# Kernel optimization log

Hardware: AMD Instinct MI355X
Metric: run time of the kernel (lower is better)

Reference implementation:

```python
import jax, jax.numpy as jnp
import numpy as np

N, IN_F, OUT_F = 2048, 512, 512

def setup_inputs() -> dict:
    key = jax.random.key(0)
    kx, ka, kb = jax.random.split(key, 3)
    x = jax.random.uniform(kx, (N, IN_F), dtype=jnp.float32)          # inputs in [0,1]
    a = jax.random.uniform(ka, (OUT_F, IN_F), dtype=jnp.float32)      # weight in [0,1]
    b = jax.random.uniform(kb, (OUT_F,), dtype=jnp.float32)           # bias in [0,1]
    return {"x": x, "a": a, "b": b}

def reference(x, a, b):
    # Lukasiewicz / max-plus 'matmul':
    # y[n,o] = max(0, max_i(x[n,i] + a[o,i] - 1)), then max with bias b[o].
    inter = x[:, None, :] + a[None, :, :] - 1.0        # [N, out, in]
    y = jnp.maximum(jnp.max(inter, axis=-1), 0.0)      # [N, out]
    y = jnp.maximum(y, b[None, :])
    return y
```

## Files before the change

### kernel.cpp

```cpp
#include <hip/hip_runtime.h>
#include <cstdint>


#define NROW 2048
#define NK   512
#define NCOL 512
#define RPB  8
#define CBL  256
#define KQ   32
typedef float f32x4 __attribute__((ext_vector_type(4)));

__device__ __forceinline__ void async_load16(const float* g, float* l) {
  __builtin_amdgcn_global_load_lds(
      (const __attribute__((address_space(1))) void*)g,
      (__attribute__((address_space(3))) void*)l, 16, 0, 0);
}

__global__ __launch_bounds__(256) void luka_prep(const float* __restrict__ A,
                                                 f32x4* __restrict__ Apb) {
  int idx = blockIdx.x * 256 + threadIdx.x;
  int o  = idx >> 7;
  int k4 = idx & 127;
  f32x4 v = *(const f32x4*)(A + o * NK + k4 * 4);
  Apb[(((o >> 8) * 128) + k4) * 256 + (o & 255)] = v;
}

__global__ __launch_bounds__(256, 2) void luka_main(
    const f32x4* __restrict__ Apb, const float* __restrict__ X,
    const float* __restrict__ Bv, float* __restrict__ Y) {
  __shared__ float xsl[RPB * NK];
  __shared__ float red[4 * RPB * CBL];
  const int tid  = threadIdx.x;
  const int lane = tid & 63;
  const int w    = tid >> 6;
  const int colblk  = blockIdx.x;
  const int rowBase = blockIdx.y * RPB;

  {
    const float* Xg = X + (size_t)rowBase * NK;
#pragma unroll
    for (int rnd = 0; rnd < 4; ++rnd) {
      int base = rnd * 256 + w * 64;
      async_load16(Xg + (size_t)(base + lane) * 4, &xsl[base * 4]);
    }
  }

  const f32x4* __restrict__ Aw =
      Apb + ((size_t)(colblk * 128 + w * KQ) * 256 + lane);

  float acc[RPB][4];
#pragma unroll
  for (int r = 0; r < RPB; ++r)
#pragma unroll
    for (int c = 0; c < 4; ++c) acc[r][c] = 0.0f;

  f32x4 a0 = Aw[0], a1 = Aw[64], a2 = Aw[128], a3 = Aw[192];

  __syncthreads();

#pragma unroll 2
  for (int j = 0; j < KQ; ++j) {
    f32x4 n0, n1, n2, n3;
    if (j + 1 < KQ) {
      n0 = Aw[(j + 1) * 256];
      n1 = Aw[(j + 1) * 256 + 64];
      n2 = Aw[(j + 1) * 256 + 128];
      n3 = Aw[(j + 1) * 256 + 192];
    }
    const int kb = (w * KQ + j) * 4;
#pragma unroll
    for (int r = 0; r < RPB; ++r) {
      const f32x4 xv = *(const f32x4*)&xsl[r * NK + kb];
      f32x4 s0 = a0 + xv;
      f32x4 s1 = a1 + xv;
      f32x4 s2 = a2 + xv;
      f32x4 s3 = a3 + xv;
      acc[r][0] = fmaxf(fmaxf(s0.x, s0.y), acc[r][0]);
      acc[r][0] = fmaxf(fmaxf(s0.z, s0.w), acc[r][0]);
      acc[r][1] = fmaxf(fmaxf(s1.x, s1.y), acc[r][1]);
      acc[r][1] = fmaxf(fmaxf(s1.z, s1.w), acc[r][1]);
      acc[r][2] = fmaxf(fmaxf(s2.x, s2.y), acc[r][2]);
      acc[r][2] = fmaxf(fmaxf(s2.z, s2.w), acc[r][2]);
      acc[r][3] = fmaxf(fmaxf(s3.x, s3.y), acc[r][3]);
      acc[r][3] = fmaxf(fmaxf(s3.z, s3.w), acc[r][3]);
    }
    a0 = n0; a1 = n1; a2 = n2; a3 = n3;
  }

#pragma unroll
  for (int r = 0; r < RPB; ++r)
#pragma unroll
    for (int c = 0; c < 4; ++c)
      red[(w * RPB + r) * CBL + c * 64 + lane] = acc[r][c];
  __syncthreads();

  const float bv = Bv[colblk * CBL + tid];
#pragma unroll
  for (int p = 0; p < RPB; ++p) {
    float m = fmaxf(fmaxf(red[(0 * RPB + p) * CBL + tid],
                          red[(1 * RPB + p) * CBL + tid]),
                    fmaxf(red[(2 * RPB + p) * CBL + tid],
                          red[(3 * RPB + p) * CBL + tid]));
    float t = m - 1.0f;
    Y[(size_t)(rowBase + p) * NCOL + colblk * CBL + tid] =
        fmaxf(fmaxf(t, bv), 0.0f);
  }
}

#define TILE 64
#define BK   64
__global__ __launch_bounds__(256) void luka_fb(
    const float* __restrict__ X, const float* __restrict__ A,
    const float* __restrict__ Bv, float* __restrict__ Y) {
  __shared__ float xs[2][TILE * BK];
  __shared__ float as[2][TILE * BK];
  const int tid = threadIdx.x, wave = tid >> 6, tx = tid & 15, ty = tid >> 4;
  const int rowBase = blockIdx.y * TILE, colBase = blockIdx.x * TILE;
  uint32_t xoff[4], aoff[4];
#pragma unroll
  for (int r = 0; r < 4; ++r) {
    int row = ty * 4 + r;
    xoff[r] = (uint32_t)row * 256u + ((uint32_t)((row & 15) ^ (row >> 2)) << 4);
  }
#pragma unroll
  for (int c = 0; c < 4; ++c) {
    int row = tx * 4 + c;
    aoff[c] = (uint32_t)row * 256u + ((uint32_t)((row & 15) ^ (row >> 2)) << 4);
  }
  float acc[4][4];
#pragma unroll
  for (int r = 0; r < 4; ++r)
#pragma unroll
    for (int c = 0; c < 4; ++c) acc[r][c] = 0.0f;
  const int row0 = tid >> 4, sl = tid & 15;
  auto stage = [&](int buf, int kt) {
#pragma unroll
    for (int j = 0; j < 4; ++j) {
      int row = row0 + j * 16;
      int m = (row & 15) ^ (row >> 2);
      int kk = ((sl ^ m) << 2);
      async_load16(X + (size_t)(rowBase + row) * NK + kt * BK + kk,
                   &xs[buf][j * 1024 + wave * 256]);
      async_load16(A + (size_t)(colBase + row) * NK + kt * BK + kk,
                   &as[buf][j * 1024 + wave * 256]);
    }
  };
  stage(0, 0);
  __syncthreads();
  int buf = 0;
#pragma unroll 1
  for (int kt = 0; kt < NK / BK; ++kt) {
    if (kt < NK / BK - 1) stage(buf ^ 1, kt + 1);
    const char* xb = (const char*)&xs[buf][0];
    const char* ab = (const char*)&as[buf][0];
#pragma unroll
    for (int s4 = 0; s4 < BK / 4; ++s4) {
      f32x4 xf[4], af[4];
#pragma unroll
      for (int r = 0; r < 4; ++r)
        xf[r] = *(const f32x4*)(xb + (xoff[r] ^ (uint32_t)(s4 << 4)));
#pragma unroll
      for (int c = 0; c < 4; ++c)
        af[c] = *(const f32x4*)(ab + (aoff[c] ^ (uint32_t)(s4 << 4)));
#pragma unroll
      for (int r = 0; r < 4; ++r)
#pragma unroll
        for (int c = 0; c < 4; ++c) {
          f32x4 s = xf[r] + af[c];
          float t0 = fmaxf(fmaxf(s.x, s.y), acc[r][c]);
          acc[r][c] = fmaxf(fmaxf(s.z, s.w), t0);
        }
    }
    __syncthreads();
    buf ^= 1;
  }
  const f32x4 bv = *(const f32x4*)&Bv[colBase + tx * 4];
  float bvv[4] = {bv.x, bv.y, bv.z, bv.w};
#pragma unroll
  for (int r = 0; r < 4; ++r) {
    f32x4 o;
    o.x = fmaxf(fmaxf(acc[r][0] - 1.0f, bvv[0]), 0.0f);
    o.y = fmaxf(fmaxf(acc[r][1] - 1.0f, bvv[1]), 0.0f);
    o.z = fmaxf(fmaxf(acc[r][2] - 1.0f, bvv[2]), 0.0f);
    o.w = fmaxf(fmaxf(acc[r][3] - 1.0f, bvv[3]), 0.0f);
    *(f32x4*)&Y[(size_t)(rowBase + ty * 4 + r) * NCOL + colBase + tx * 4] = o;
  }
}

extern "C" void kernel_launch(void* const* d_in, const int* in_sizes, int n_in,
                              void* d_out, int out_size, void* d_ws, size_t ws_size,
                              hipStream_t stream) {
  const float* X = (const float*)d_in[0];
  const float* A = (const float*)d_in[1];
  const float* B = (const float*)d_in[2];
  float* Y = (float*)d_out;

  if (ws_size >= (size_t)NCOL * NK * sizeof(float)) {
    f32x4* Apb = (f32x4*)d_ws;
    luka_prep<<<dim3(NCOL * NK / 4 / 256), dim3(256), 0, stream>>>(A, Apb);
    dim3 grid(NCOL / CBL, NROW / RPB);
    luka_main<<<grid, dim3(256), 0, stream>>>(Apb, X, B, Y);
  } else {
    dim3 grid(NCOL / TILE, NROW / TILE);
    luka_fb<<<grid, dim3(256), 0, stream>>>(X, A, B, Y);
  }
}
```

Before: 83.75 us.

## Interleave prepacked weight columns per lane and use nontemporal loads

The prep kernel now stores the four column-chunks each lane needs next to each other, so every thread reads 64 contiguous bytes per k-step instead of four strided 16-byte vectors. The main kernel reads the weights with nontemporal loads and drops the min-blocks-per-CU launch bound. This aims to cut memory transactions and cache pollution on the weight stream. The per-wave access becomes a 64-byte stride per lane, which may coalesce less well, and nontemporal hints may hurt reuse of A across row blocks.

```diff
diff --git a/kernel.cpp b/kernel.cpp
--- a/kernel.cpp
+++ b/kernel.cpp
@@ -17,16 +17,18 @@
 }
 
 __global__ __launch_bounds__(256) void luka_prep(const float* __restrict__ A,
-                                                 f32x4* __restrict__ Apb) {
+                                                 f32x4* __restrict__ Apc) {
   int idx = blockIdx.x * 256 + threadIdx.x;
   int o  = idx >> 7;
   int k4 = idx & 127;
+  int cb = o >> 8, oc = o & 255;
+  int c  = oc >> 6, l = oc & 63;
   f32x4 v = *(const f32x4*)(A + o * NK + k4 * 4);
-  Apb[(((o >> 8) * 128) + k4) * 256 + (o & 255)] = v;
-}
-
-__global__ __launch_bounds__(256, 2) void luka_main(
-    const f32x4* __restrict__ Apb, const float* __restrict__ X,
+  Apc[((cb * 128 + k4) << 8) + (l << 2) + c] = v;
+}
+
+__global__ __launch_bounds__(256) void luka_main(
+    const f32x4* __restrict__ Apc, const float* __restrict__ X,
     const float* __restrict__ Bv, float* __restrict__ Y) {
   __shared__ float xsl[RPB * NK];
   __shared__ float red[4 * RPB * CBL];
@@ -46,7 +48,7 @@
   }
 
   const f32x4* __restrict__ Aw =
-      Apb + ((size_t)(colblk * 128 + w * KQ) * 256 + lane);
+      Apc + (((size_t)(colblk * 128 + w * KQ)) << 8) + (lane << 2);
 
   float acc[RPB][4];
 #pragma unroll
@@ -54,7 +56,10 @@
 #pragma unroll
     for (int c = 0; c < 4; ++c) acc[r][c] = 0.0f;
 
-  f32x4 a0 = Aw[0], a1 = Aw[64], a2 = Aw[128], a3 = Aw[192];
+  f32x4 a0 = __builtin_nontemporal_load(Aw + 0);
+  f32x4 a1 = __builtin_nontemporal_load(Aw + 1);
+  f32x4 a2 = __builtin_nontemporal_load(Aw + 2);
+  f32x4 a3 = __builtin_nontemporal_load(Aw + 3);
 
   __syncthreads();
 
@@ -62,10 +67,11 @@
   for (int j = 0; j < KQ; ++j) {
     f32x4 n0, n1, n2, n3;
     if (j + 1 < KQ) {
-      n0 = Aw[(j + 1) * 256];
-      n1 = Aw[(j + 1) * 256 + 64];
-      n2 = Aw[(j + 1) * 256 + 128];
-      n3 = Aw[(j + 1) * 256 + 192];
+      const f32x4* p = Aw + ((j + 1) << 8);
+      n0 = __builtin_nontemporal_load(p + 0);
+      n1 = __builtin_nontemporal_load(p + 1);
+      n2 = __builtin_nontemporal_load(p + 2);
+      n3 = __builtin_nontemporal_load(p + 3);
     }
     const int kb = (w * KQ + j) * 4;
 #pragma unroll
@@ -196,10 +202,10 @@
   float* Y = (float*)d_out;
 
   if (ws_size >= (size_t)NCOL * NK * sizeof(float)) {
-    f32x4* Apb = (f32x4*)d_ws;
-    luka_prep<<<dim3(NCOL * NK / 4 / 256), dim3(256), 0, stream>>>(A, Apb);
+    f32x4* Apc = (f32x4*)d_ws;
+    luka_prep<<<dim3(NCOL * NK / 4 / 256), dim3(256), 0, stream>>>(A, Apc);
     dim3 grid(NCOL / CBL, NROW / RPB);
-    luka_main<<<grid, dim3(256), 0, stream>>>(Apb, X, B, Y);
+    luka_main<<<grid, dim3(256), 0, stream>>>(Apc, X, B, Y);
   } else {
     dim3 grid(NCOL / TILE, NROW / TILE);
     luka_fb<<<grid, dim3(256), 0, stream>>>(X, A, B, Y);
```

New measurement: 99.41 us. +18.7%, slower.
